# Kernel optimization log

Measured on AMD Instinct MI355X. Metric: run time of the kernel, lower is better.

## Reference

```python
import jax, jax.numpy as jnp
import numpy as np

DIM = 256      # block dim
NH = 4         # num_head
HD = DIM // 2  # head_dim = dim // 2 (per CrossBlock -> CroA)
HALF = DIM // 2  # channels per axial branch
DI = NH * HD   # inner qkv dim = 512
B, H, W = 8, 56, 56


def _conv1x1(w, b, x):
    # 1x1 conv == per-pixel channel matmul; w:[Cout,Cin], x:[B,Cin,H,W]
    return jnp.einsum('oc,bchw->bohw', w, x) + b[None, :, None, None]


def _mha(x, qw, qb, kw, kb, vw, vb, pw, pb, rel):
    # axial MHA over the last (W) axis, per row, matching torch MHA exactly
    Bx, C, Hx, Wx = x.shape
    q = _conv1x1(qw, qb, x).transpose(0, 2, 1, 3).reshape(Bx, Hx, NH, HD, Wx)
    k = _conv1x1(kw, kb, x).transpose(0, 2, 1, 3).reshape(Bx, Hx, NH, HD, Wx)
    v = _conv1x1(vw, vb, x).transpose(0, 2, 1, 3).reshape(Bx, Hx, NH, HD, Wx)
    att = jnp.einsum('bhndi,bhndj->bhnij', q, k) * (HD ** -0.5)
    L = Wx
    # gathered relative-position bias (RelPos); torch does this under no_grad
    idx = (jnp.arange(L)[:, None] - jnp.arange(L)[None, :] + L - 1).reshape(-1)
    bias = jax.lax.stop_gradient(rel[:, idx].reshape(NH, L, L))
    att = jax.nn.softmax(att + bias[None, None], axis=-1)
    out = jnp.einsum('bhnij,bhndj->bhnid', att, v)  # [B,H,nh,W,hd]
    # faithful to torch: raw reshape of [B*H, nh, W, hd] -> (B, H, W, nh*hd)
    out = out.reshape(Bx, Hx, Wx, NH * HD).transpose(0, 3, 1, 2)
    return _conv1x1(pw, pb, out) + x


def _forward(x, xq_w, xq_b, xk_w, xk_b, xv_w, xv_b, xp_w, xp_b, rel_x,
             yq_w, yq_b, yk_w, yk_b, yv_w, yv_b, yp_w, yp_b, rel_y,
             cp_w, cp_b, m1_w, m1_b, m2_w, m2_b, ls1, ls2):
    ax, ay = jnp.split(x, 2, axis=1)
    ax = _mha(ax, xq_w, xq_b, xk_w, xk_b, xv_w, xv_b, xp_w, xp_b, rel_x)
    ay = _mha(ay.transpose(0, 1, 3, 2), yq_w, yq_b, yk_w, yk_b, yv_w, yv_b,
              yp_w, yp_b, rel_y).transpose(0, 1, 3, 2)
    net = _conv1x1(cp_w, cp_b, jnp.concatenate([ax, ay], axis=1))
    net = net * ls1[None] + x                      # layer_scale1 + residual
    h = jax.nn.gelu(_conv1x1(m1_w, m1_b, net), approximate=False)
    out = _conv1x1(m2_w, m2_b, h)
    return out * ls2[None] + net                   # layer_scale2 + identity skip (dim==out_dim)


def setup_inputs() -> dict:
    key = jax.random.key(0)
    ks = iter(jax.random.split(key, 32))
    def w(shape, s=0.05):
        return jax.random.normal(next(ks), shape, dtype=jnp.float32) * s
    return dict(
        x=jax.random.normal(next(ks), (B, DIM, H, W), dtype=jnp.float32),
        xq_w=w((DI, HALF)), xq_b=w((DI,)), xk_w=w((DI, HALF)), xk_b=w((DI,)),
        xv_w=w((DI, HALF)), xv_b=w((DI,)), xp_w=w((HALF, DI)), xp_b=w((HALF,)),
        rel_x=jax.random.normal(next(ks), (NH, W * W), dtype=jnp.float32),
        yq_w=w((DI, HALF)), yq_b=w((DI,)), yk_w=w((DI, HALF)), yk_b=w((DI,)),
        yv_w=w((DI, HALF)), yv_b=w((DI,)), yp_w=w((HALF, DI)), yp_b=w((HALF,)),
        rel_y=jax.random.normal(next(ks), (NH, H * H), dtype=jnp.float32),
        cp_w=w((DIM, DIM)), cp_b=w((DIM,)),
        m1_w=w((2 * DIM, DIM)), m1_b=w((2 * DIM,)),
        m2_w=w((DIM, 2 * DIM)), m2_b=w((DIM,)),
        ls1=jnp.ones((DIM, 1, 1), jnp.float32),
        ls2=jnp.ones((DIM, 1, 1), jnp.float32),
    )


def reference(x, xq_w, xq_b, xk_w, xk_b, xv_w, xv_b, xp_w, xp_b, rel_x,
              yq_w, yq_b, yk_w, yk_b, yv_w, yv_b, yp_w, yp_b, rel_y,
              cp_w, cp_b, m1_w, m1_b, m2_w, m2_b, ls1, ls2):
    return _forward(x, xq_w, xq_b, xk_w, xk_b, xv_w, xv_b, xp_w, xp_b, rel_x,
                    yq_w, yq_b, yk_w, yk_b, yv_w, yv_b, yp_w, yp_b, rel_y,
                    cp_w, cp_b, m1_w, m1_b, m2_w, m2_b, ls1, ls2)
```

## Files before the change

### kernel.cpp

```cpp
#include <hip/hip_runtime.h>

using u16 = unsigned short;
using u32 = unsigned int;

typedef short bf16x8 __attribute__((ext_vector_type(8)));
typedef float f32x4 __attribute__((ext_vector_type(4)));

#define HW 3136
#define IMG 56

__device__ __forceinline__ float bf2f(u16 v) {
    union { u32 u; float f; } c; c.u = ((u32)v) << 16; return c.f;
}
__device__ __forceinline__ u16 f2bf(float f) {
    union { float f; u32 u; } c; c.f = f;
    return (u16)((c.u + 0x7fffu + ((c.u >> 16) & 1u)) >> 16);
}
__device__ __forceinline__ u32 pk2bf(float a, float b) {
    u32 r;
    asm("v_cvt_pk_bf16_f32 %0, %1, %2" : "=v"(r) : "v"(a), "v"(b));
    return r;
}
__device__ __forceinline__ int swz8(int r) { return (r ^ (r >> 3)) & 7; }

__device__ __forceinline__ f32x4 mfma16(bf16x8 a, bf16x8 b, f32x4 c) {
    return __builtin_amdgcn_mfma_f32_16x16x32_bf16(a, b, c, 0, 0, 0);
}

__device__ __forceinline__ void gl_lds(const void* g, void* l) {
    __builtin_amdgcn_global_load_lds((const __attribute__((address_space(1))) void*)g,
                                     (__attribute__((address_space(3))) void*)l, 16, 0, 0);
}

__global__ __launch_bounds__(256) void wcvt(
    const float* __restrict__ s0, const float* __restrict__ s1, const float* __restrict__ s2,
    const float* __restrict__ s3, const float* __restrict__ s4, const float* __restrict__ s5,
    const float* __restrict__ s6, const float* __restrict__ s7, const float* __restrict__ s8,
    const float* __restrict__ s9, const float* __restrict__ s10,
    const float* __restrict__ b0, const float* __restrict__ b1, const float* __restrict__ b2,
    const float* __restrict__ b3, const float* __restrict__ b4, const float* __restrict__ b5,
    const float* __restrict__ b6, const float* __restrict__ b7, const float* __restrict__ b8,
    const float* __restrict__ b9, const float* __restrict__ b10,
    u16* __restrict__ Wb, float* __restrict__ Bc)
{
    const int tid = threadIdx.x;
    if (blockIdx.x == 832) {
        for (int i = tid; i < 4352; i += 256) {
            const float* src; int off;
            if      (i < 512)  { src = b0;  off = i; }
            else if (i < 1024) { src = b1;  off = i - 512; }
            else if (i < 1536) { src = b2;  off = i - 1024; }
            else if (i < 2048) { src = b3;  off = i - 1536; }
            else if (i < 2560) { src = b4;  off = i - 2048; }
            else if (i < 3072) { src = b5;  off = i - 2560; }
            else if (i < 3200) { src = b6;  off = i - 3072; }
            else if (i < 3328) { src = b7;  off = i - 3200; }
            else if (i < 3584) { src = b8;  off = i - 3328; }
            else if (i < 4096) { src = b9;  off = i - 3584; }
            else               { src = b10; off = i - 4096; }
            Bc[i] = src[off];
        }
        return;
    }
    long gid4 = ((long)blockIdx.x * 256 + tid) * 4;
    const float* src; long off;
    if (gid4 < 589824) {
        int seg = (int)(gid4 >> 16);
        const float* tab[9] = { s0, s1, s2, s3, s4, s5, s6, s7, s8 };
        src = tab[seg]; off = gid4 - ((long)seg << 16);
    } else if (gid4 < 720896) { src = s9;  off = gid4 - 589824; }
    else                      { src = s10; off = gid4 - 720896; }
    float4 v = *(const float4*)(src + off);
    *(uint2*)(Wb + gid4) = make_uint2(pk2bf(v.x, v.y), pk2bf(v.z, v.w));
}

__global__ __launch_bounds__(256) void transpose_x(
    const float* __restrict__ x, u16* __restrict__ Xt)
{
    __shared__ u16 lds[64][80];
    const int t = threadIdx.x;
    const int Pb = blockIdx.x * 64;
    const int Cb = blockIdx.y * 64;
    const int b  = blockIdx.z;

    #pragma unroll
    for (int q = 0; q < 4; ++q) {
        int id = t + q * 256;
        int c = id >> 4, pf = (id & 15) * 4;
        float4 v = *(const float4*)(x + ((long)(b * 256 + Cb + c)) * HW + Pb + pf);
        u16 vv[4] = { f2bf(v.x), f2bf(v.y), f2bf(v.z), f2bf(v.w) };
        #pragma unroll
        for (int j = 0; j < 4; ++j) {
            int p = pf + j;
            int cc = (((c >> 3) ^ ((p >> 2) & 7)) << 3) + (c & 7);
            lds[p][cc] = vv[j];
        }
    }
    __syncthreads();
    int p = t >> 2, cf = (t & 3) * 16;
    u16* dst = Xt + ((long)b * HW + Pb + p) * 256 + Cb + cf;
    int cc0 = ((cf >> 3) + 0) ^ ((p >> 2) & 7);
    int cc1 = ((cf >> 3) + 1) ^ ((p >> 2) & 7);
    *(uint4*)(dst + 0) = *(uint4*)&lds[p][cc0 * 8];
    *(uint4*)(dst + 8) = *(uint4*)&lds[p][cc1 * 8];
}

__global__ __launch_bounds__(256, 2) void fused_attn(
    const u16* __restrict__ Wb, const float* __restrict__ Bc,
    const u16* __restrict__ Xt,
    const float* __restrict__ rel_x, const float* __restrict__ rel_y,
    u16* __restrict__ SbX, u16* __restrict__ SbY)
{
    __shared__ __align__(16) char smem[66048];
    const int tid = threadIdx.x;
    const int lane = tid & 63, wid = tid >> 6;
    const int l15 = lane & 15, lg = lane >> 4;

    const int g = blockIdx.x;
    const int n = blockIdx.y;
    const int branch = blockIdx.z >> 3;
    const int b = blockIdx.z & 7;

    const float* rel = branch ? rel_y : rel_x;
    u16* S = branch ? SbY : SbX;
    const u16* wsrc = Wb + branch * 196608 + n * 16384;
    const float* bsrc = Bc + branch * 1536 + n * 128;

    if (tid < 128) {
        float v = (tid < 112) ? rel[n * HW + tid] : 0.0f;
        *(float*)(smem + 65536 + tid * 4) = v;
    }

    bf16x8 wf[3][2][4];
    #pragma unroll
    for (int mat = 0; mat < 3; ++mat)
        #pragma unroll
        for (int mt = 0; mt < 2; ++mt) {
            int mrow = (wid * 2 + mt) * 16 + l15;
            const u16* wr = wsrc + mat * 65536 + mrow * 128;
            #pragma unroll
            for (int ks = 0; ks < 4; ++ks)
                wf[mat][mt][ks] = *(const bf16x8*)(wr + (ks * 4 + lg) * 8);
        }
    float4 bq4[2], bk4[2]; float bvv[2];
    #pragma unroll
    for (int mt = 0; mt < 2; ++mt) {
        int m0 = (wid * 2 + mt) * 16 + lg * 4;
        bq4[mt] = *(const float4*)(bsrc + m0);
        bk4[mt] = *(const float4*)(bsrc + 512 + m0);
        bvv[mt] = bsrc[1024 + (wid * 2 + mt) * 16 + l15];
    }

    const int istrip = wid * 16;
    const float qscale = 0.08838834764831845f;

    auto stageX = [&](int rc2) {
        const int i0 = wid * 16 + (lane >> 4);
        #pragma unroll
        for (int t = 0; t < 4; ++t) {
            int i = i0 + t * 4;
            int ic = (i > 55) ? 55 : i;
            long p = (branch == 0) ? (long)rc2 * IMG + ic : (long)ic * IMG + rc2;
            const u16* src = Xt + ((long)b * HW + p) * 256 + branch * 128
                             + (((lane & 15) ^ swz8(i)) * 8);
            gl_lds(src, smem + 49152 + wid * 4096 + t * 1024);
        }
    };

    stageX(g * 7);

    for (int r = 0; r < 7; ++r) {
        const int rc = g * 7 + r;

        __syncthreads();

        bf16x8 xf[4][4];
        #pragma unroll
        for (int it = 0; it < 4; ++it) {
            int i = it * 16 + l15;
            #pragma unroll
            for (int ks = 0; ks < 4; ++ks)
                xf[it][ks] = *(const bf16x8*)(smem + 49152 + i * 256
                                              + (((ks * 4 + lg) ^ swz8(i)) * 16));
        }

        #pragma unroll
        for (int mat = 0; mat < 2; ++mat) {
            #pragma unroll
            for (int mt = 0; mt < 2; ++mt) {
                #pragma unroll
                for (int it = 0; it < 4; ++it) {
                    f32x4 a = {};
                    #pragma unroll
                    for (int ks = 0; ks < 4; ++ks)
                        a = mfma16(wf[mat][mt][ks], xf[it][ks], a);
                    int i = it * 16 + l15;
                    int m0 = (wid * 2 + mt) * 16 + lg * 4;
                    float4 bb2 = mat ? bk4[mt] : bq4[mt];
                    int c = m0 >> 3;
                    *(uint2*)(smem + mat * 16384 + i * 256 + ((c ^ swz8(i)) * 16) + (lg & 1) * 8)
                        = make_uint2(pk2bf(a[0] + bb2.x, a[1] + bb2.y),
                                     pk2bf(a[2] + bb2.z, a[3] + bb2.w));
                }
            }
        }
        #pragma unroll
        for (int mt = 0; mt < 2; ++mt) {
            #pragma unroll
            for (int it = 0; it < 4; ++it) {
                f32x4 a = {};
                #pragma unroll
                for (int ks = 0; ks < 4; ++ks)
                    a = mfma16(xf[it][ks], wf[2][mt][ks], a);
                int d = (wid * 2 + mt) * 16 + l15;
                int c2 = (it >> 1) * 4 + lg;
                float bv = bvv[mt];
                *(uint2*)(smem + 32768 + d * 128 + ((c2 ^ swz8(d)) * 16) + (it & 1) * 8)
                    = make_uint2(pk2bf(a[0] + bv, a[1] + bv),
                                 pk2bf(a[2] + bv, a[3] + bv));
            }
        }
        __syncthreads();

        if (r < 6) stageX(rc + 1);

        bf16x8 aq[4];
        #pragma unroll
        for (int ks = 0; ks < 4; ++ks) {
            int row = istrip + l15;
            int ch = ks * 4 + lg;
            aq[ks] = *(const bf16x8*)(smem + row * 256 + ((ch ^ swz8(row)) * 16));
        }
        f32x4 sacc[4] = {};
        #pragma unroll
        for (int ct = 0; ct < 4; ++ct) {
            #pragma unroll
            for (int ks = 0; ks < 4; ++ks) {
                int j = ct * 16 + l15;
                int ch = ks * 4 + lg;
                bf16x8 kb = *(const bf16x8*)(smem + 16384 + j * 256 + ((ch ^ swz8(j)) * 16));
                sacc[ct] = mfma16(kb, aq[ks], sacc[ct]);
            }
        }

        const int irow = istrip + l15;
        float p[4][4];
        float mx = -1e30f;
        #pragma unroll
        for (int ct = 0; ct < 4; ++ct)
            #pragma unroll
            for (int rr = 0; rr < 4; ++rr) {
                int j = ct * 16 + lg * 4 + rr;
                float x = sacc[ct][rr] * qscale;
                if (j < IMG) x += *(const float*)(smem + 65536 + (irow - j + 55) * 4);
                else x = -1e30f;
                p[ct][rr] = x;
                mx = fmaxf(mx, x);
            }
        mx = fmaxf(mx, __shfl_xor(mx, 16));
        mx = fmaxf(mx, __shfl_xor(mx, 32));
        float s0 = 0.f;
        #pragma unroll
        for (int ct = 0; ct < 4; ++ct)
            #pragma unroll
            for (int rr = 0; rr < 4; ++rr) {
                float e = __expf(p[ct][rr] - mx);
                p[ct][rr] = e; s0 += e;
            }
        s0 += __shfl_xor(s0, 16);
        s0 += __shfl_xor(s0, 32);
        float inv = 1.0f / s0;

        union { u32 u[4]; bf16x8 v; } pb[2];
        #pragma unroll
        for (int ks = 0; ks < 2; ++ks) {
            pb[ks].u[0] = pk2bf(p[2*ks][0] * inv, p[2*ks][1] * inv);
            pb[ks].u[1] = pk2bf(p[2*ks][2] * inv, p[2*ks][3] * inv);
            pb[ks].u[2] = pk2bf(p[2*ks+1][0] * inv, p[2*ks+1][1] * inv);
            pb[ks].u[3] = pk2bf(p[2*ks+1][2] * inv, p[2*ks+1][3] * inv);
        }

        f32x4 oacc[8] = {};
        #pragma unroll
        for (int dt = 0; dt < 8; ++dt) {
            #pragma unroll
            for (int ks = 0; ks < 2; ++ks) {
                int d = dt * 16 + l15;
                int c2 = ks * 4 + lg;
                bf16x8 vb = *(const bf16x8*)(smem + 32768 + d * 128 + ((c2 ^ swz8(d)) * 16));
                oacc[dt] = mfma16(vb, pb[ks].v, oacc[dt]);
            }
        }

        const int i = istrip + l15;
        if (i < IMG) {
            int im = n * 14 + (i >> 2);
            long pp = (branch == 0) ? (long)rc * IMG + im : (long)im * IMG + rc;
            u16* dst = S + ((long)b * HW + pp) * 512 + (i & 3) * 128;
            #pragma unroll
            for (int dt = 0; dt < 8; ++dt) {
                int d4 = dt * 16 + lg * 4;
                *(uint2*)(dst + d4) = make_uint2(pk2bf(oacc[dt][0], oacc[dt][1]),
                                                 pk2bf(oacc[dt][2], oacc[dt][3]));
            }
        }
    }
}

__global__ __launch_bounds__(256, 2) void opcp(
    const u16* __restrict__ Wb, const float* __restrict__ Bc,
    const u16* __restrict__ SbX, const u16* __restrict__ SbY,
    const u16* __restrict__ Xt, const float* __restrict__ ls1,
    u16* __restrict__ NETp)
{
    __shared__ __align__(16) char smem[81920];
    const int tid = threadIdx.x;
    const int lane = tid & 63, wid = tid >> 6;
    const int l15 = lane & 15, lg = lane >> 4;
    const int P0 = blockIdx.x * 64;
    const int b  = blockIdx.z;

    const u16* xp = Wb + 393216;
    const u16* yp = Wb + 458752;
    const u16* cpw = Wb + 524288;

    f32x4 acc[4][4] = {};

    for (int ko = 0; ko < 512; ko += 64) {
        #pragma unroll
        for (int t = 0; t < 2; ++t) {
            int row = wid * 16 + t * 8 + (lane >> 3);
            int c = (lane & 7) ^ swz8(row);
            long prow = (long)b * HW + P0 + row;
            gl_lds(SbX + prow * 512 + ko + c * 8, smem + wid * 2048 + t * 1024);
            gl_lds(SbY + prow * 512 + ko + c * 8, smem + 8192 + wid * 2048 + t * 1024);
        }
        #pragma unroll
        for (int t = 0; t < 4; ++t) {
            int row = wid * 32 + t * 8 + (lane >> 3);
            int c = (lane & 7) ^ swz8(row);
            gl_lds(xp + (long)row * 512 + ko + c * 8, smem + 16384 + wid * 4096 + t * 1024);
            gl_lds(yp + (long)row * 512 + ko + c * 8, smem + 32768 + wid * 4096 + t * 1024);
        }
        __syncthreads();

        const int actb = (wid < 2) ? 0 : 8192;
        const int wbse = (wid < 2) ? 16384 : 32768;
        const int wrow0 = (wid & 1) * 64;
        #pragma unroll
        for (int ks = 0; ks < 2; ++ks) {
            int ch = ks * 4 + lg;
            bf16x8 af[4], bfr[4];
            #pragma unroll
            for (int rt = 0; rt < 4; ++rt) {
                int row = rt * 16 + l15;
                af[rt] = *(const bf16x8*)(smem + actb + row * 128 + ((ch ^ swz8(row)) * 16));
            }
            #pragma unroll
            for (int ct = 0; ct < 4; ++ct) {
                int row = wrow0 + ct * 16 + l15;
                bfr[ct] = *(const bf16x8*)(smem + wbse + row * 128 + ((ch ^ swz8(row)) * 16));
            }
            #pragma unroll
            for (int rt = 0; rt < 4; ++rt)
                #pragma unroll
                for (int ct = 0; ct < 4; ++ct)
                    acc[rt][ct] = mfma16(bfr[ct], af[rt], acc[rt][ct]);
        }
        __syncthreads();
    }

    #pragma unroll
    for (int rt = 0; rt < 4; ++rt) {
        int pl = rt * 16 + l15;
        long rowp = (long)b * HW + P0 + pl;
        #pragma unroll
        for (int ct = 0; ct < 4; ++ct) {
            int mg2 = wid * 64 + ct * 16 + lg * 4;
            float4 bv = *(const float4*)(Bc + 3072 + mg2);
            ushort4 rv = *(const ushort4*)(Xt + rowp * 256 + mg2);
            float v0 = acc[rt][ct][0] + bv.x + bf2f(rv.x);
            float v1 = acc[rt][ct][1] + bv.y + bf2f(rv.y);
            float v2 = acc[rt][ct][2] + bv.z + bf2f(rv.z);
            float v3 = acc[rt][ct][3] + bv.w + bf2f(rv.w);
            int cc = mg2 >> 3;
            int pos = (cc & 24) | ((cc ^ swz8(pl)) & 7);
            *(uint2*)(smem + 49152 + pl * 512 + pos * 16 + (mg2 & 7) * 2)
                = make_uint2(pk2bf(v0, v1), pk2bf(v2, v3));
        }
    }
    __syncthreads();

    f32x4 acc2[4][4] = {};
    for (int ko = 0; ko < 256; ko += 64) {
        #pragma unroll
        for (int t = 0; t < 8; ++t) {
            int row = wid * 64 + t * 8 + (lane >> 3);
            int c = (lane & 7) ^ swz8(row);
            gl_lds(cpw + (long)row * 256 + ko + c * 8, smem + 16384 + wid * 8192 + t * 1024);
        }
        __syncthreads();

        #pragma unroll
        for (int ks = 0; ks < 2; ++ks) {
            int ch = ks * 4 + lg;
            bf16x8 af[4], bfr[4];
            #pragma unroll
            for (int rt = 0; rt < 4; ++rt) {
                int row = rt * 16 + l15;
                int c = (ko >> 3) + ch;
                int pos = (c & 24) | ((c ^ swz8(row)) & 7);
                af[rt] = *(const bf16x8*)(smem + 49152 + row * 512 + pos * 16);
            }
            #pragma unroll
            for (int ct = 0; ct < 4; ++ct) {
                int row = wid * 64 + ct * 16 + l15;
                bfr[ct] = *(const bf16x8*)(smem + 16384 + row * 128 + ((ch ^ swz8(row)) * 16));
            }
            #pragma unroll
            for (int rt = 0; rt < 4; ++rt)
                #pragma unroll
                for (int ct = 0; ct < 4; ++ct)
                    acc2[rt][ct] = mfma16(bfr[ct], af[rt], acc2[rt][ct]);
        }
        __syncthreads();
    }

    #pragma unroll
    for (int rt = 0; rt < 4; ++rt) {
        int pl = rt * 16 + l15;
        long rowp = (long)b * HW + P0 + pl;
        #pragma unroll
        for (int ct = 0; ct < 4; ++ct) {
            int mg = wid * 64 + ct * 16 + lg * 4;
            float4 bv = *(const float4*)(Bc + 3328 + mg);
            float4 sv = *(const float4*)(ls1 + mg);
            ushort4 rv = *(const ushort4*)(Xt + rowp * 256 + mg);
            float v0 = (acc2[rt][ct][0] + bv.x) * sv.x + bf2f(rv.x);
            float v1 = (acc2[rt][ct][1] + bv.y) * sv.y + bf2f(rv.y);
            float v2 = (acc2[rt][ct][2] + bv.z) * sv.z + bf2f(rv.z);
            float v3 = (acc2[rt][ct][3] + bv.w) * sv.w + bf2f(rv.w);
            *(uint2*)(NETp + rowp * 256 + mg) = make_uint2(pk2bf(v0, v1), pk2bf(v2, v3));
        }
    }
}

__global__ __launch_bounds__(256, 2) void mlp(
    const u16* __restrict__ Wb, const float* __restrict__ Bc,
    const u16* __restrict__ NETp, const float* __restrict__ ls2,
    u16* __restrict__ OUTp)
{
    __shared__ __align__(16) char smem[81920];
    const int tid = threadIdx.x;
    const int lane = tid & 63, wid = tid >> 6;
    const int l15 = lane & 15, lg = lane >> 4;
    const int P0 = blockIdx.x * 64;
    const int b  = blockIdx.z;

    const u16* m1w = Wb + 589824;
    const u16* m2w = Wb + 720896;

    #pragma unroll
    for (int t = 0; t < 8; ++t) {
        int row = wid * 16 + t * 2 + (lane >> 5);
        int cc = lane & 31;
        int sc = (cc & 24) | ((cc ^ swz8(row)) & 7);
        gl_lds(NETp + ((long)b * HW + P0 + row) * 256 + sc * 8,
               smem + wid * 8192 + t * 1024);
    }

    f32x4 aco[4][4] = {};

    for (int hc = 0; hc < 4; ++hc) {
        f32x4 ach[4][2] = {};
        for (int ko = 0; ko < 256; ko += 64) {
            #pragma unroll
            for (int t = 0; t < 4; ++t) {
                int row = wid * 32 + t * 8 + (lane >> 3);
                int c = (lane & 7) ^ swz8(row);
                gl_lds(m1w + (long)(hc * 128 + row) * 256 + ko + c * 8,
                       smem + 49152 + wid * 4096 + t * 1024);
            }
            __syncthreads();

            #pragma unroll
            for (int ks = 0; ks < 2; ++ks) {
                int ch = ks * 4 + lg;
                bf16x8 af[4], bfrh[2];
                #pragma unroll
                for (int rt = 0; rt < 4; ++rt) {
                    int row = rt * 16 + l15;
                    int c = (ko >> 3) + ch;
                    int pos = (c & 24) | ((c ^ swz8(row)) & 7);
                    af[rt] = *(const bf16x8*)(smem + row * 512 + pos * 16);
                }
                #pragma unroll
                for (int mt = 0; mt < 2; ++mt) {
                    int row = wid * 32 + mt * 16 + l15;
                    bfrh[mt] = *(const bf16x8*)(smem + 49152 + row * 128 + ((ch ^ swz8(row)) * 16));
                }
                #pragma unroll
                for (int rt = 0; rt < 4; ++rt)
                    #pragma unroll
                    for (int mt = 0; mt < 2; ++mt)
                        ach[rt][mt] = mfma16(bfrh[mt], af[rt], ach[rt][mt]);
            }
            __syncthreads();
        }
        #pragma unroll
        for (int rt = 0; rt < 4; ++rt) {
            int pl = rt * 16 + l15;
            #pragma unroll
            for (int mt = 0; mt < 2; ++mt) {
                int hloc = wid * 32 + mt * 16 + lg * 4;
                float4 bv = *(const float4*)(Bc + 3584 + hc * 128 + hloc);
                float v[4];
                #pragma unroll
                for (int j = 0; j < 4; ++j) {
                    float tt = ach[rt][mt][j] + ((const float*)&bv)[j];
                    v[j] = tt * 0.5f * (1.0f + erff(tt * 0.70710678118f));
                }
                int cc = hloc >> 3;
                int pos = (cc & 8) | ((cc ^ swz8(pl)) & 7);
                *(uint2*)(smem + 32768 + pl * 256 + pos * 16 + (hloc & 7) * 2)
                    = make_uint2(pk2bf(v[0], v[1]), pk2bf(v[2], v[3]));
            }
        }

        for (int ko = 0; ko < 128; ko += 64) {
            #pragma unroll
            for (int t = 0; t < 8; ++t) {
                int row = wid * 64 + t * 8 + (lane >> 3);
                int c = (lane & 7) ^ swz8(row);
                gl_lds(m2w + (long)row * 512 + hc * 128 + ko + c * 8,
                       smem + 49152 + wid * 8192 + t * 1024);
            }
            __syncthreads();

            #pragma unroll
            for (int ks = 0; ks < 2; ++ks) {
                int ch = ks * 4 + lg;
                bf16x8 af[4], bfr[4];
                #pragma unroll
                for (int rt = 0; rt < 4; ++rt) {
                    int row = rt * 16 + l15;
                    int c = (ko >> 3) + ch;
                    int pos = (c & 8) | ((c ^ swz8(row)) & 7);
                    af[rt] = *(const bf16x8*)(smem + 32768 + row * 256 + pos * 16);
                }
                #pragma unroll
                for (int ct = 0; ct < 4; ++ct) {
                    int row = wid * 64 + ct * 16 + l15;
                    bfr[ct] = *(const bf16x8*)(smem + 49152 + row * 128 + ((ch ^ swz8(row)) * 16));
                }
                #pragma unroll
                for (int rt = 0; rt < 4; ++rt)
                    #pragma unroll
                    for (int ct = 0; ct < 4; ++ct)
                        aco[rt][ct] = mfma16(bfr[ct], af[rt], aco[rt][ct]);
            }
            __syncthreads();
        }
    }

    #pragma unroll
    for (int rt = 0; rt < 4; ++rt) {
        int pl = rt * 16 + l15;
        long rowp = (long)b * HW + P0 + pl;
        #pragma unroll
        for (int ct = 0; ct < 4; ++ct) {
            int mg = wid * 64 + ct * 16 + lg * 4;
            float4 bv = *(const float4*)(Bc + 4096 + mg);
            float4 sv = *(const float4*)(ls2 + mg);
            int cc = mg >> 3;
            int pos = (cc & 24) | ((cc ^ swz8(pl)) & 7);
            uint2 nv2 = *(const uint2*)(smem + pl * 512 + pos * 16 + (mg & 7) * 2);
            u16 nv[4] = { (u16)(nv2.x & 0xffff), (u16)(nv2.x >> 16),
                          (u16)(nv2.y & 0xffff), (u16)(nv2.y >> 16) };
            float v0 = (aco[rt][ct][0] + bv.x) * sv.x + bf2f(nv[0]);
            float v1 = (aco[rt][ct][1] + bv.y) * sv.y + bf2f(nv[1]);
            float v2 = (aco[rt][ct][2] + bv.z) * sv.z + bf2f(nv[2]);
            float v3 = (aco[rt][ct][3] + bv.w) * sv.w + bf2f(nv[3]);
            *(uint2*)(OUTp + rowp * 256 + mg) = make_uint2(pk2bf(v0, v1), pk2bf(v2, v3));
        }
    }
}

__global__ __launch_bounds__(256) void fuse_out(
    const u16* __restrict__ OUTp, float* __restrict__ y)
{
    __shared__ float lds[32][132];
    const int t = threadIdx.x;
    const int Pb = blockIdx.x * 128;
    const int Cb = blockIdx.y * 32;
    const int b  = blockIdx.z;

    #pragma unroll
    for (int q = 0; q < 4; ++q) {
        int id = t + q * 256;
        int p = id >> 3, cq = (id & 7) * 4;
        int pg = Pb + p;
        float4 v = make_float4(0.f, 0.f, 0.f, 0.f);
        if (pg < HW) {
            ushort4 nv = *(const ushort4*)(OUTp + ((long)b * HW + pg) * 256 + Cb + cq);
            v.x = bf2f(nv.x); v.y = bf2f(nv.y); v.z = bf2f(nv.z); v.w = bf2f(nv.w);
        }
        lds[cq + 0][p] = v.x; lds[cq + 1][p] = v.y;
        lds[cq + 2][p] = v.z; lds[cq + 3][p] = v.w;
    }
    __syncthreads();
    #pragma unroll
    for (int q = 0; q < 4; ++q) {
        int id = t + q * 256;
        int c = id >> 5, pq = (id & 31) * 4;
        int pg = Pb + pq;
        if (pg + 3 < HW) {
            float4 v = make_float4(lds[c][pq], lds[c][pq + 1], lds[c][pq + 2], lds[c][pq + 3]);
            *(float4*)(y + ((long)(b * 256 + Cb + c)) * HW + pg) = v;
        }
    }
}

extern "C" void kernel_launch(void* const* d_in, const int* in_sizes, int n_in,
                              void* d_out, int out_size, void* d_ws, size_t ws_size,
                              hipStream_t stream)
{
    const float* x     = (const float*)d_in[0];
    const float* xq_w  = (const float*)d_in[1];
    const float* xq_b  = (const float*)d_in[2];
    const float* xk_w  = (const float*)d_in[3];
    const float* xk_b  = (const float*)d_in[4];
    const float* xv_w  = (const float*)d_in[5];
    const float* xv_b  = (const float*)d_in[6];
    const float* xp_w  = (const float*)d_in[7];
    const float* xp_b  = (const float*)d_in[8];
    const float* rel_x = (const float*)d_in[9];
    const float* yq_w  = (const float*)d_in[10];
    const float* yq_b  = (const float*)d_in[11];
    const float* yk_w  = (const float*)d_in[12];
    const float* yk_b  = (const float*)d_in[13];
    const float* yv_w  = (const float*)d_in[14];
    const float* yv_b  = (const float*)d_in[15];
    const float* yp_w  = (const float*)d_in[16];
    const float* yp_b  = (const float*)d_in[17];
    const float* rel_y = (const float*)d_in[18];
    const float* cp_w  = (const float*)d_in[19];
    const float* cp_b  = (const float*)d_in[20];
    const float* m1_w  = (const float*)d_in[21];
    const float* m1_b  = (const float*)d_in[22];
    const float* m2_w  = (const float*)d_in[23];
    const float* m2_b  = (const float*)d_in[24];
    const float* ls1   = (const float*)d_in[25];
    const float* ls2   = (const float*)d_in[26];

    if (ws_size < 128450560) return;

    char* ws = (char*)d_ws;
    u16*   SbY  = (u16*)(ws + 0);
    u16*   OUTp = (u16*)(ws + 25690112);
    u16*   Xt   = (u16*)(ws + 77070336);
    u16*   SbX  = (u16*)(ws + 89915392);
    u16*   NETp = (u16*)(ws + 115605504);

    u16*   Wb = (u16*)d_out;
    float* Bc = (float*)((char*)d_out + 1703936);

    dim3 blk(256, 1, 1);

    wcvt<<<dim3(833, 1, 1), blk, 0, stream>>>(
        xq_w, xk_w, xv_w, yq_w, yk_w, yv_w, xp_w, yp_w, cp_w, m1_w, m2_w,
        xq_b, xk_b, xv_b, yq_b, yk_b, yv_b, xp_b, yp_b, cp_b, m1_b, m2_b,
        Wb, Bc);
    transpose_x<<<dim3(49, 4, 8), blk, 0, stream>>>(x, Xt);
    fused_attn<<<dim3(8, 4, 16), blk, 0, stream>>>(Wb, Bc, Xt, rel_x, rel_y, SbX, SbY);
    opcp<<<dim3(49, 1, 8), blk, 0, stream>>>(Wb, Bc, SbX, SbY, Xt, ls1, NETp);
    mlp<<<dim3(49, 1, 8), blk, 0, stream>>>(Wb, Bc, NETp, ls2, OUTp);
    fuse_out<<<dim3(25, 8, 8), blk, 0, stream>>>(OUTp, (float*)d_out);
}
```

Baseline: 148.2 us.

## Merge weight-convert with x transpose, and fuse proj/cp with MLP in one kernel

Combines the weight conversion and input transpose into a single prep launch, and merges the opcp and mlp kernels so the post-residual activation stays in shared memory instead of round-tripping through a global NETp buffer. Shared memory regions are remapped so the net tile, the m1/m2 weight tiles and the hidden tile coexist within the 80KB budget. This removes two launches and a global write and read of the intermediate, in exchange for a longer-running kernel with more register and LDS pressure at the same grid size.

```diff
diff --git a/kernel.cpp b/kernel.cpp
--- a/kernel.cpp
+++ b/kernel.cpp
@@ -32,7 +32,8 @@
                                      (__attribute__((address_space(3))) void*)l, 16, 0, 0);
 }
 
-__global__ __launch_bounds__(256) void wcvt(
+__global__ __launch_bounds__(256) void prep(
+    const float* __restrict__ x, u16* __restrict__ Xt,
     const float* __restrict__ s0, const float* __restrict__ s1, const float* __restrict__ s2,
     const float* __restrict__ s3, const float* __restrict__ s4, const float* __restrict__ s5,
     const float* __restrict__ s6, const float* __restrict__ s7, const float* __restrict__ s8,
@@ -43,9 +44,40 @@
     const float* __restrict__ b9, const float* __restrict__ b10,
     u16* __restrict__ Wb, float* __restrict__ Bc)
 {
-    const int tid = threadIdx.x;
-    if (blockIdx.x == 832) {
-        for (int i = tid; i < 4352; i += 256) {
+    __shared__ u16 lds[64][80];
+    const int t = threadIdx.x;
+    const int idx = blockIdx.x;
+
+    if (idx < 1568) {
+        const int Pb = (idx % 49) * 64;
+        const int Cb = ((idx / 49) & 3) * 64;
+        const int b  = idx / 196;
+        #pragma unroll
+        for (int q = 0; q < 4; ++q) {
+            int id = t + q * 256;
+            int c = id >> 4, pf = (id & 15) * 4;
+            float4 v = *(const float4*)(x + ((long)(b * 256 + Cb + c)) * HW + Pb + pf);
+            u16 vv[4] = { f2bf(v.x), f2bf(v.y), f2bf(v.z), f2bf(v.w) };
+            #pragma unroll
+            for (int j = 0; j < 4; ++j) {
+                int p = pf + j;
+                int cc = (((c >> 3) ^ ((p >> 2) & 7)) << 3) + (c & 7);
+                lds[p][cc] = vv[j];
+            }
+        }
+        __syncthreads();
+        int p = t >> 2, cf = (t & 3) * 16;
+        u16* dst = Xt + ((long)b * HW + Pb + p) * 256 + Cb + cf;
+        int cc0 = ((cf >> 3) + 0) ^ ((p >> 2) & 7);
+        int cc1 = ((cf >> 3) + 1) ^ ((p >> 2) & 7);
+        *(uint4*)(dst + 0) = *(uint4*)&lds[p][cc0 * 8];
+        *(uint4*)(dst + 8) = *(uint4*)&lds[p][cc1 * 8];
+        return;
+    }
+
+    const int bx = idx - 1568;
+    if (bx == 832) {
+        for (int i = t; i < 4352; i += 256) {
             const float* src; int off;
             if      (i < 512)  { src = b0;  off = i; }
             else if (i < 1024) { src = b1;  off = i - 512; }
@@ -62,7 +94,7 @@
         }
         return;
     }
-    long gid4 = ((long)blockIdx.x * 256 + tid) * 4;
+    long gid4 = ((long)bx * 256 + t) * 4;
     const float* src; long off;
     if (gid4 < 589824) {
         int seg = (int)(gid4 >> 16);
@@ -72,37 +104,6 @@
     else                      { src = s10; off = gid4 - 720896; }
     float4 v = *(const float4*)(src + off);
     *(uint2*)(Wb + gid4) = make_uint2(pk2bf(v.x, v.y), pk2bf(v.z, v.w));
-}
-
-__global__ __launch_bounds__(256) void transpose_x(
-    const float* __restrict__ x, u16* __restrict__ Xt)
-{
-    __shared__ u16 lds[64][80];
-    const int t = threadIdx.x;
-    const int Pb = blockIdx.x * 64;
-    const int Cb = blockIdx.y * 64;
-    const int b  = blockIdx.z;
-
-    #pragma unroll
-    for (int q = 0; q < 4; ++q) {
-        int id = t + q * 256;
-        int c = id >> 4, pf = (id & 15) * 4;
-        float4 v = *(const float4*)(x + ((long)(b * 256 + Cb + c)) * HW + Pb + pf);
-        u16 vv[4] = { f2bf(v.x), f2bf(v.y), f2bf(v.z), f2bf(v.w) };
-        #pragma unroll
-        for (int j = 0; j < 4; ++j) {
-            int p = pf + j;
-            int cc = (((c >> 3) ^ ((p >> 2) & 7)) << 3) + (c & 7);
-            lds[p][cc] = vv[j];
-        }
-    }
-    __syncthreads();
-    int p = t >> 2, cf = (t & 3) * 16;
-    u16* dst = Xt + ((long)b * HW + Pb + p) * 256 + Cb + cf;
-    int cc0 = ((cf >> 3) + 0) ^ ((p >> 2) & 7);
-    int cc1 = ((cf >> 3) + 1) ^ ((p >> 2) & 7);
-    *(uint4*)(dst + 0) = *(uint4*)&lds[p][cc0 * 8];
-    *(uint4*)(dst + 8) = *(uint4*)&lds[p][cc1 * 8];
 }
 
 __global__ __launch_bounds__(256, 2) void fused_attn(
@@ -307,11 +308,12 @@
     }
 }
 
-__global__ __launch_bounds__(256, 2) void opcp(
+__global__ __launch_bounds__(256, 2) void tail(
     const u16* __restrict__ Wb, const float* __restrict__ Bc,
     const u16* __restrict__ SbX, const u16* __restrict__ SbY,
-    const u16* __restrict__ Xt, const float* __restrict__ ls1,
-    u16* __restrict__ NETp)
+    const u16* __restrict__ Xt,
+    const float* __restrict__ ls1, const float* __restrict__ ls2,
+    u16* __restrict__ OUTp)
 {
     __shared__ __align__(16) char smem[81920];
     const int tid = threadIdx.x;
@@ -320,12 +322,13 @@
     const int P0 = blockIdx.x * 64;
     const int b  = blockIdx.z;
 
-    const u16* xp = Wb + 393216;
-    const u16* yp = Wb + 458752;
+    const u16* xp  = Wb + 393216;
+    const u16* yp  = Wb + 458752;
     const u16* cpw = Wb + 524288;
+    const u16* m1w = Wb + 589824;
+    const u16* m2w = Wb + 720896;
 
     f32x4 acc[4][4] = {};
-
     for (int ko = 0; ko < 512; ko += 64) {
         #pragma unroll
         for (int t = 0; t < 2; ++t) {
@@ -440,33 +443,11 @@
             float v1 = (acc2[rt][ct][1] + bv.y) * sv.y + bf2f(rv.y);
             float v2 = (acc2[rt][ct][2] + bv.z) * sv.z + bf2f(rv.z);
             float v3 = (acc2[rt][ct][3] + bv.w) * sv.w + bf2f(rv.w);
-            *(uint2*)(NETp + rowp * 256 + mg) = make_uint2(pk2bf(v0, v1), pk2bf(v2, v3));
-        }
-    }
-}
-
-__global__ __launch_bounds__(256, 2) void mlp(
-    const u16* __restrict__ Wb, const float* __restrict__ Bc,
-    const u16* __restrict__ NETp, const float* __restrict__ ls2,
-    u16* __restrict__ OUTp)
-{
-    __shared__ __align__(16) char smem[81920];
-    const int tid = threadIdx.x;
-    const int lane = tid & 63, wid = tid >> 6;
-    const int l15 = lane & 15, lg = lane >> 4;
-    const int P0 = blockIdx.x * 64;
-    const int b  = blockIdx.z;
-
-    const u16* m1w = Wb + 589824;
-    const u16* m2w = Wb + 720896;
-
-    #pragma unroll
-    for (int t = 0; t < 8; ++t) {
-        int row = wid * 16 + t * 2 + (lane >> 5);
-        int cc = lane & 31;
-        int sc = (cc & 24) | ((cc ^ swz8(row)) & 7);
-        gl_lds(NETp + ((long)b * HW + P0 + row) * 256 + sc * 8,
-               smem + wid * 8192 + t * 1024);
+            int cc = mg >> 3;
+            int pos = (cc & 24) | ((cc ^ swz8(pl)) & 7);
+            *(uint2*)(smem + 16384 + pl * 512 + pos * 16 + (mg & 7) * 2)
+                = make_uint2(pk2bf(v0, v1), pk2bf(v2, v3));
+        }
     }
 
     f32x4 aco[4][4] = {};
@@ -479,7 +460,7 @@
                 int row = wid * 32 + t * 8 + (lane >> 3);
                 int c = (lane & 7) ^ swz8(row);
                 gl_lds(m1w + (long)(hc * 128 + row) * 256 + ko + c * 8,
-                       smem + 49152 + wid * 4096 + t * 1024);
+                       smem + wid * 4096 + t * 1024);
             }
             __syncthreads();
 
@@ -492,12 +473,12 @@
                     int row = rt * 16 + l15;
                     int c = (ko >> 3) + ch;
                     int pos = (c & 24) | ((c ^ swz8(row)) & 7);
-                    af[rt] = *(const bf16x8*)(smem + row * 512 + pos * 16);
+                    af[rt] = *(const bf16x8*)(smem + 16384 + row * 512 + pos * 16);
                 }
                 #pragma unroll
                 for (int mt = 0; mt < 2; ++mt) {
                     int row = wid * 32 + mt * 16 + l15;
-                    bfrh[mt] = *(const bf16x8*)(smem + 49152 + row * 128 + ((ch ^ swz8(row)) * 16));
+                    bfrh[mt] = *(const bf16x8*)(smem + row * 128 + ((ch ^ swz8(row)) * 16));
                 }
                 #pragma unroll
                 for (int rt = 0; rt < 4; ++rt)
@@ -522,7 +503,7 @@
                 }
                 int cc = hloc >> 3;
                 int pos = (cc & 8) | ((cc ^ swz8(pl)) & 7);
-                *(uint2*)(smem + 32768 + pl * 256 + pos * 16 + (hloc & 7) * 2)
+                *(uint2*)(smem + 49152 + pl * 256 + pos * 16 + (hloc & 7) * 2)
                     = make_uint2(pk2bf(v[0], v[1]), pk2bf(v[2], v[3]));
             }
         }
@@ -532,8 +513,9 @@
             for (int t = 0; t < 8; ++t) {
                 int row = wid * 64 + t * 8 + (lane >> 3);
                 int c = (lane & 7) ^ swz8(row);
-                gl_lds(m2w + (long)row * 512 + hc * 128 + ko + c * 8,
-                       smem + 49152 + wid * 8192 + t * 1024);
+                char* dst = ((wid < 2) ? (smem + wid * 8192) : (smem + 65536 + (wid - 2) * 8192))
+                            + t * 1024;
+                gl_lds(m2w + (long)row * 512 + hc * 128 + ko + c * 8, dst);
             }
             __syncthreads();
 
@@ -546,12 +528,13 @@
                     int row = rt * 16 + l15;
                     int c = (ko >> 3) + ch;
                     int pos = (c & 8) | ((c ^ swz8(row)) & 7);
-                    af[rt] = *(const bf16x8*)(smem + 32768 + row * 256 + pos * 16);
+                    af[rt] = *(const bf16x8*)(smem + 49152 + row * 256 + pos * 16);
                 }
                 #pragma unroll
                 for (int ct = 0; ct < 4; ++ct) {
                     int row = wid * 64 + ct * 16 + l15;
-                    bfr[ct] = *(const bf16x8*)(smem + 49152 + row * 128 + ((ch ^ swz8(row)) * 16));
+                    const char* base = (wid < 2) ? smem : (smem + 65536 - 16384);
+                    bfr[ct] = *(const bf16x8*)(base + row * 128 + ((ch ^ swz8(row)) * 16));
                 }
                 #pragma unroll
                 for (int rt = 0; rt < 4; ++rt)
@@ -574,7 +557,7 @@
             float4 sv = *(const float4*)(ls2 + mg);
             int cc = mg >> 3;
             int pos = (cc & 24) | ((cc ^ swz8(pl)) & 7);
-            uint2 nv2 = *(const uint2*)(smem + pl * 512 + pos * 16 + (mg & 7) * 2);
+            uint2 nv2 = *(const uint2*)(smem + 16384 + pl * 512 + pos * 16 + (mg & 7) * 2);
             u16 nv[4] = { (u16)(nv2.x & 0xffff), (u16)(nv2.x >> 16),
                           (u16)(nv2.y & 0xffff), (u16)(nv2.y >> 16) };
             float v0 = (aco[rt][ct][0] + bv.x) * sv.x + bf2f(nv[0]);
@@ -660,20 +643,18 @@
     u16*   OUTp = (u16*)(ws + 25690112);
     u16*   Xt   = (u16*)(ws + 77070336);
     u16*   SbX  = (u16*)(ws + 89915392);
-    u16*   NETp = (u16*)(ws + 115605504);
 
     u16*   Wb = (u16*)d_out;
     float* Bc = (float*)((char*)d_out + 1703936);
 
     dim3 blk(256, 1, 1);
 
-    wcvt<<<dim3(833, 1, 1), blk, 0, stream>>>(
+    prep<<<dim3(2401, 1, 1), blk, 0, stream>>>(
+        x, Xt,
         xq_w, xk_w, xv_w, yq_w, yk_w, yv_w, xp_w, yp_w, cp_w, m1_w, m2_w,
         xq_b, xk_b, xv_b, yq_b, yk_b, yv_b, xp_b, yp_b, cp_b, m1_b, m2_b,
         Wb, Bc);
-    transpose_x<<<dim3(49, 4, 8), blk, 0, stream>>>(x, Xt);
     fused_attn<<<dim3(8, 4, 16), blk, 0, stream>>>(Wb, Bc, Xt, rel_x, rel_y, SbX, SbY);
-    opcp<<<dim3(49, 1, 8), blk, 0, stream>>>(Wb, Bc, SbX, SbY, Xt, ls1, NETp);
-    mlp<<<dim3(49, 1, 8), blk, 0, stream>>>(Wb, Bc, NETp, ls2, OUTp);
+    tail<<<dim3(49, 1, 8), blk, 0, stream>>>(Wb, Bc, SbX, SbY, Xt, ls1, ls2, OUTp);
     fuse_out<<<dim3(25, 8, 8), blk, 0, stream>>>(OUTp, (float*)d_out);
 }
```

After: 136.5 us. -7.9%, faster.
